# Kernel optimization log

Measured on AMD Instinct MI355X. Metric: run time of the kernel, lower is better.

The kernel has to match this reference:

```python
import jax, jax.numpy as jnp
import numpy as np

N, B, NPG = 65536, 512, 128      # total nodes, graphs, nodes per graph
E, EPG = 524288, 1024            # total edges, edges per graph
D, R, L = 64, 16, 3              # emb_dim, num relations, encoder layers
PHI = 0.1
EPS_VAR = 1e-5


def _mean_std(x):
    # torch.var is unbiased (ddof=1); keep last-dim stats per row
    m = jnp.mean(x, axis=-1, keepdims=True)
    s = jnp.sqrt(jnp.var(x, axis=-1, ddof=1, keepdims=True) + EPS_VAR)
    return m, s


def _rgcn_encode(feat, Wrel, Wself, b, src, dst, etype, edge_w):
    """L-layer relational GCN. Returns (last_h [N,D], repr [N,L,D])."""
    h = feat
    reps = []
    for l in range(L):
        hr = jnp.einsum('nd,rdk->nrk', h, Wrel[l])        # [N,R,D]
        msg = hr[src, etype]                               # [E,D] per-edge typed transform
        msg = msg * edge_w[:, None]
        agg = jax.ops.segment_sum(msg, dst, num_segments=N)
        deg = jax.ops.segment_sum(edge_w, dst, num_segments=N)
        h = jax.nn.relu(h @ Wself[l] + agg / jnp.clip(deg, 1.0)[:, None] + b[l])
        reps.append(h)
    return h, jnp.stack(reps, axis=1)


def _pool(rep, node_gid):
    # mean_nodes over 'repr': graphs have fixed NPG nodes
    s = jax.ops.segment_sum(rep.reshape(N, L * D), node_gid, num_segments=B)
    return (s / NPG).reshape(B, L, D)


def full_forward(feat, rel_feat, rel_proj_W, rel_proj_b, rgcn_Wrel, rgcn_Wself,
                 rgcn_b, enc_W_mean, enc_W_std, dec_Wh, dec_bh, dec_Wt, dec_bt,
                 dec_Wr, dec_br, fc_W, fc_b, eps,
                 src, dst, etype, aug_src, aug_dst, aug_etype, node_gid, rel_labels):
    ones_e = jnp.ones((E,), feat.dtype)
    # relation encoder + projection
    emb_rel = jax.nn.relu(rel_feat @ rel_proj_W + rel_proj_b)          # [R,D]
    # encode original and augmented graphs
    x, rep_g = _rgcn_encode(feat, rgcn_Wrel, rgcn_Wself, rgcn_b, src, dst, etype, ones_e)
    g_out = _pool(rep_g, node_gid)
    aug_x, rep_aug = _rgcn_encode(feat, rgcn_Wrel, rgcn_Wself, rgcn_b, aug_src, aug_dst, aug_etype, ones_e)
    aug_g_out = _pool(rep_aug, node_gid)
    # AdaIn style transfer (args.interp == False)
    mc, sc = _mean_std(x)
    ms, ss = _mean_std(aug_x)
    style_applied = ss * ((x - mc) / sc) + ms
    # VAE reparameterization
    z_mean = style_applied @ enc_W_mean
    z_std = style_applied @ enc_W_std
    z = z_mean + jnp.sqrt(jnp.exp(z_std)) * eps
    # decoder: edge-level DistMult scoring -> edge mask
    head_e = jax.nn.relu(z[src] @ dec_Wh + dec_bh)                     # [E,D]
    tail_e = jax.nn.relu(z[dst] @ dec_Wt + dec_bt)
    rel_e = jax.nn.relu(emb_rel[etype] @ dec_Wr + dec_br)
    logit = jnp.sum(head_e * rel_e * tail_e, axis=-1)                  # [E]
    mask = (logit >= 0.5).astype(feat.dtype)
    # root edge (edge_ids(0,1)) = first edge of each graph, forced kept
    mask = mask.at[jnp.arange(B) * EPG].set(1.0)
    # re-encode reconstructed (masked) graph with original features
    x_recon, rep_recon = _rgcn_encode(feat, rgcn_Wrel, rgcn_Wself, rgcn_b, src, dst, etype, mask)
    recon_g_out = _pool(rep_recon, node_gid)
    # head node (id==1) = node 0 of each graph; tail (id==2) = node 1
    head_ids = jnp.arange(B) * NPG
    tail_ids = head_ids + 1
    g_rep = jnp.concatenate([
        recon_g_out.reshape(B, L * D),
        rep_recon[head_ids].reshape(B, L * D),
        rep_recon[tail_ids].reshape(B, L * D),
        emb_rel[rel_labels],
    ], axis=1)                                                          # [B, 3*L*D + D]
    output = g_rep @ fc_W + fc_b                                        # [B,1]
    # reconstruction + style losses, summed over layers
    mse_per_layer = jnp.mean((rep_recon - rep_g) ** 2, axis=(0, 2))     # [L]
    mr, sr = _mean_std(rep_recon.transpose(1, 0, 2))                    # [L,N,1]
    mg, sg = _mean_std(rep_g.transpose(1, 0, 2))
    style_per_layer = jnp.mean((mr - mg) ** 2, axis=(1, 2)) + jnp.mean((sr - sg) ** 2, axis=(1, 2))
    loss = jnp.sum(mse_per_layer) + PHI * jnp.sum(style_per_layer)
    return output, g_out, aug_g_out, loss


def setup_inputs() -> dict:
    key = jax.random.key(0)
    ks = jax.random.split(key, 28)
    egid = jnp.arange(E, dtype=jnp.int32) // EPG
    node_gid = jnp.arange(N, dtype=jnp.int32) // NPG
    mk_edges = lambda k1, k2: (egid * NPG + jax.random.randint(k1, (E,), 0, NPG, jnp.int32),
                               egid * NPG + jax.random.randint(k2, (E,), 0, NPG, jnp.int32))
    src, dst = mk_edges(ks[0], ks[1])
    aug_src, aug_dst = mk_edges(ks[2], ks[3])
    g = lambda i, shape, s=0.05: (jax.random.normal(ks[i], shape, jnp.float32) * s)
    return {
        'feat': g(4, (N, D), 1.0),
        'rel_feat': g(5, (R, 64), 1.0),
        'rel_proj_W': g(6, (64, D)),
        'rel_proj_b': jnp.zeros((D,), jnp.float32),
        'rgcn_Wrel': g(7, (L, R, D, D)),
        'rgcn_Wself': g(8, (L, D, D)),
        'rgcn_b': jnp.zeros((L, D), jnp.float32),
        'enc_W_mean': g(9, (D, D)),
        'enc_W_std': g(10, (D, D)),
        'dec_Wh': g(11, (D, D), 0.1),
        'dec_bh': jnp.zeros((D,), jnp.float32),
        'dec_Wt': g(12, (D, D), 0.1),
        'dec_bt': jnp.zeros((D,), jnp.float32),
        'dec_Wr': g(13, (D, D), 0.1),
        'dec_br': jnp.zeros((D,), jnp.float32),
        'fc_W': g(14, (3 * L * D + D, 1)),
        'fc_b': jnp.zeros((1,), jnp.float32),
        'eps': g(15, (N, D), 1.0),
        'src': src, 'dst': dst,
        'etype': jax.random.randint(ks[16], (E,), 0, R, jnp.int32),
        'aug_src': aug_src, 'aug_dst': aug_dst,
        'aug_etype': jax.random.randint(ks[17], (E,), 0, R, jnp.int32),
        'node_gid': node_gid,
        'rel_labels': jax.random.randint(ks[18], (B,), 0, R, jnp.int32),
    }


def reference(feat, rel_feat, rel_proj_W, rel_proj_b, rgcn_Wrel, rgcn_Wself,
              rgcn_b, enc_W_mean, enc_W_std, dec_Wh, dec_bh, dec_Wt, dec_bt,
              dec_Wr, dec_br, fc_W, fc_b, eps,
              src, dst, etype, aug_src, aug_dst, aug_etype, node_gid, rel_labels):
    return full_forward(feat, rel_feat, rel_proj_W, rel_proj_b, rgcn_Wrel, rgcn_Wself,
                        rgcn_b, enc_W_mean, enc_W_std, dec_Wh, dec_bh, dec_Wt, dec_bt,
                        dec_Wr, dec_br, fc_W, fc_b, eps,
                        src, dst, etype, aug_src, aug_dst, aug_etype, node_gid, rel_labels)
```

## Files before the change

kernel.cpp:

```cpp
#include <hip/hip_runtime.h>
#include <hip/hip_bf16.h>

typedef __attribute__((ext_vector_type(8))) short bf16x8;
typedef __attribute__((ext_vector_type(4))) float f32x4;

#define NPG  128
#define EPG  1024
#define BG   512
#define NT   512
#define NW   8
#define PHI  0.1f
#define EPSV 1e-5f
#define SB   72
#define SF   65

#define OUT_G    512
#define OUT_AUG  98816
#define OUT_LOSS 197120
#define WS_EMB   0
#define WS_RELE  1024
#define WS_REPG  2048

__device__ __forceinline__ unsigned short f2bf(float x) {
  __hip_bfloat16 h = __float2bfloat16(x);
  return *reinterpret_cast<unsigned short*>(&h);
}
__device__ __forceinline__ float bf2f(unsigned short u) {
  __hip_bfloat16 h = *reinterpret_cast<__hip_bfloat16*>(&u);
  return __bfloat162float(h);
}
__device__ __forceinline__ void split_write(unsigned short* hh, unsigned short* hl,
                                            int idx, float x) {
  unsigned short hi = f2bf(x);
  hh[idx] = hi;
  hl[idx] = f2bf(x - bf2f(hi));
}

#define LOAD_BF(Wp, ctn, ks, bhv, blv)                                         \
  {                                                                            \
    bf16x8 h_, l_;                                                             \
    _Pragma("unroll") for (int j_ = 0; j_ < 8; j_++) {                         \
      float w_ = (Wp)[((ks) * 32 + kg * 8 + j_) * 64 + (ctn) * 16 + n];        \
      unsigned short hi_ = f2bf(w_);                                           \
      h_[j_] = (short)hi_;                                                     \
      l_[j_] = (short)f2bf(w_ - bf2f(hi_));                                    \
    }                                                                          \
    bhv = h_;                                                                  \
    blv = l_;                                                                  \
  }

__device__ __forceinline__ f32x4 mfma3(bf16x8 a0h, bf16x8 a1h, bf16x8 a0l, bf16x8 a1l,
                                       bf16x8 b0h, bf16x8 b1h, bf16x8 b0l, bf16x8 b1l,
                                       f32x4 acc) {
  acc = __builtin_amdgcn_mfma_f32_16x16x32_bf16(a0h, b0h, acc, 0, 0, 0);
  acc = __builtin_amdgcn_mfma_f32_16x16x32_bf16(a1h, b1h, acc, 0, 0, 0);
  acc = __builtin_amdgcn_mfma_f32_16x16x32_bf16(a0h, b0l, acc, 0, 0, 0);
  acc = __builtin_amdgcn_mfma_f32_16x16x32_bf16(a1h, b1l, acc, 0, 0, 0);
  acc = __builtin_amdgcn_mfma_f32_16x16x32_bf16(a0l, b0h, acc, 0, 0, 0);
  acc = __builtin_amdgcn_mfma_f32_16x16x32_bf16(a1l, b1h, acc, 0, 0, 0);
  return acc;
}

__global__ __launch_bounds__(64) void k_prologue1(
    const float* __restrict__ rel_feat, const float* __restrict__ rpW,
    const float* __restrict__ rpb, float* __restrict__ ws, float* __restrict__ out) {
  int r = blockIdx.x, j = threadIdx.x;
  float s = rpb[j];
  for (int k = 0; k < 64; k++) s = fmaf(rel_feat[r * 64 + k], rpW[k * 64 + j], s);
  ws[WS_EMB + r * 64 + j] = fmaxf(s, 0.f);
  if (r == 0 && j == 0) out[OUT_LOSS] = 0.f;
}

__global__ __launch_bounds__(64) void k_prologue2(
    const float* __restrict__ dWr, const float* __restrict__ dbr,
    float* __restrict__ ws) {
  int r = blockIdx.x, j = threadIdx.x;
  float s = dbr[j];
  for (int k = 0; k < 64; k++) s = fmaf(ws[WS_EMB + r * 64 + k], dWr[k * 64 + j], s);
  ws[WS_RELE + r * 64 + j] = fmaxf(s, 0.f);
}

__device__ void build_elist(unsigned* elist, int* cnt, int* offs, int* asg, int* wload,
                            float* dinv, const unsigned* maskbits, int useMask,
                            const int* __restrict__ et_a, const int* __restrict__ src_a,
                            const int* __restrict__ dst_a, int ge, int gn, int tid) {
  if (tid < 16) cnt[tid] = 0;
  if (tid >= 128 && tid < 256) dinv[tid - 128] = 0.f;
  __syncthreads();
  for (int i = tid; i < EPG; i += NT) {
    int keep = useMask ? (int)((maskbits[i >> 5] >> (i & 31)) & 1u) : 1;
    if (keep) {
      atomicAdd(&cnt[et_a[ge + i]], 1);
      atomicAdd(&dinv[dst_a[ge + i] - gn], 1.f);
    }
  }
  __syncthreads();
  if (tid == 0) {
    int o = 0;
    for (int r = 0; r < 16; r++) { offs[r] = o; o += (cnt[r] + 15) & ~15; }
    offs[16] = o;
    for (int w = 0; w < NW; w++) wload[w] = 0;
    unsigned used = 0;
    for (int s = 0; s < 16; s++) {
      int best = 0, bc = -1;
      for (int r = 0; r < 16; r++)
        if (!((used >> r) & 1) && cnt[r] > bc) { bc = cnt[r]; best = r; }
      used |= 1u << best;
      int bw = 0;
      for (int w = 1; w < NW; w++) if (wload[w] < wload[bw]) bw = w;
      asg[best] = bw;
      wload[bw] += (bc + 15) & ~15;
    }
  }
  if (tid >= 128 && tid < 256) {
    int v = tid - 128;
    dinv[v] = 1.0f / fmaxf(dinv[v], 1.0f);
  }
  __syncthreads();
  int total = offs[16];
  for (int s = tid; s < total; s += NT) elist[s] = 128u;
  if (tid < 16) cnt[tid] = offs[tid];
  __syncthreads();
  for (int i = tid; i < EPG; i += NT) {
    int keep = useMask ? (int)((maskbits[i >> 5] >> (i & 31)) & 1u) : 1;
    if (keep) {
      int r = et_a[ge + i];
      int pos = atomicAdd(&cnt[r], 1);
      elist[pos] = ((unsigned)(src_a[ge + i] - gn) << 8) | (unsigned)(dst_a[ge + i] - gn);
    }
  }
  __syncthreads();
}

__device__ void rgcn_layer_mfma(unsigned short* hh, unsigned short* hl, float* hf32,
                                const float* dinv, const unsigned* elist,
                                const int* offs, const int* asg,
                                const float* __restrict__ Wl,
                                const float* __restrict__ Wsl,
                                const float* __restrict__ bl, int tid) {
  int lane = tid & 63, wave = tid >> 6;
  int n = lane & 15, kg = lane >> 4;
  for (int i = tid; i < NPG * SF; i += NT) hf32[i] = 0.f;
  __syncthreads();
  for (int r = 0; r < 16; r++) {
    if (asg[r] != wave) continue;
    int base = offs[r], end = offs[r + 1];
    if (base >= end) continue;
    const float* __restrict__ W = Wl + (r << 12);
#pragma unroll 1
    for (int ch = 0; ch < 2; ch++) {
      bf16x8 bh00, bh01, bl00, bl01, bh10, bh11, bl10, bl11;
      LOAD_BF(W, ch * 2 + 0, 0, bh00, bl00);
      LOAD_BF(W, ch * 2 + 0, 1, bh01, bl01);
      LOAD_BF(W, ch * 2 + 1, 0, bh10, bl10);
      LOAD_BF(W, ch * 2 + 1, 1, bh11, bl11);
      for (int tb = base; tb < end; tb += 16) {
        int srow = (int)(elist[tb + n] >> 8);
        const unsigned short* rh = hh + srow * SB;
        const unsigned short* rl = hl + srow * SB;
        bf16x8 a0h = *(const bf16x8*)(rh + kg * 8);
        bf16x8 a1h = *(const bf16x8*)(rh + 32 + kg * 8);
        bf16x8 a0l = *(const bf16x8*)(rl + kg * 8);
        bf16x8 a1l = *(const bf16x8*)(rl + 32 + kg * 8);
        f32x4 acc0 = {0.f, 0.f, 0.f, 0.f}, acc1 = {0.f, 0.f, 0.f, 0.f};
        acc0 = mfma3(a0h, a1h, a0l, a1l, bh00, bh01, bl00, bl01, acc0);
        acc1 = mfma3(a0h, a1h, a0l, a1l, bh10, bh11, bl10, bl11, acc1);
#pragma unroll
        for (int i = 0; i < 4; i++) {
          int dst = (int)(elist[tb + kg * 4 + i] & 255u);
          if (dst < 128) {
            float* hp = hf32 + dst * SF + ch * 32 + n;
            atomicAdd(hp, acc0[i]);
            atomicAdd(hp + 16, acc1[i]);
          }
        }
      }
    }
  }
  __syncthreads();
  {
    const unsigned short* rh = hh + (wave * 16 + n) * SB;
    const unsigned short* rl = hl + (wave * 16 + n) * SB;
    bf16x8 a0h = *(const bf16x8*)(rh + kg * 8);
    bf16x8 a1h = *(const bf16x8*)(rh + 32 + kg * 8);
    bf16x8 a0l = *(const bf16x8*)(rl + kg * 8);
    bf16x8 a1l = *(const bf16x8*)(rl + 32 + kg * 8);
#pragma unroll 1
    for (int ch = 0; ch < 2; ch++) {
      bf16x8 bh00, bh01, bl00, bl01, bh10, bh11, bl10, bl11;
      LOAD_BF(Wsl, ch * 2 + 0, 0, bh00, bl00);
      LOAD_BF(Wsl, ch * 2 + 0, 1, bh01, bl01);
      LOAD_BF(Wsl, ch * 2 + 1, 0, bh10, bl10);
      LOAD_BF(Wsl, ch * 2 + 1, 1, bh11, bl11);
      f32x4 acc0 = {0.f, 0.f, 0.f, 0.f}, acc1 = {0.f, 0.f, 0.f, 0.f};
      acc0 = mfma3(a0h, a1h, a0l, a1l, bh00, bh01, bl00, bl01, acc0);
      acc1 = mfma3(a0h, a1h, a0l, a1l, bh10, bh11, bl10, bl11, acc1);
#pragma unroll
      for (int i = 0; i < 4; i++) {
        int node = wave * 16 + kg * 4 + i;
        float di = dinv[node];
#pragma unroll
        for (int c = 0; c < 2; c++) {
          int col = (ch * 2 + c) * 16 + n;
          float a = c ? acc1[i] : acc0[i];
          float v = a + hf32[node * SF + col] * di + bl[col];
          v = fmaxf(v, 0.f);
          hf32[node * SF + col] = v;
          split_write(hh, hl, node * SB + col, v);
        }
      }
    }
  }
  __syncthreads();
}

__device__ void dense_mfma(const unsigned short* ah, const unsigned short* al,
                           float* hf32, unsigned short* oh, unsigned short* ol,
                           const float* __restrict__ W, const float* __restrict__ bias,
                           int mode, const float* __restrict__ epsbuf, int gn, int tid) {
  int lane = tid & 63, wave = tid >> 6;
  int n = lane & 15, kg = lane >> 4;
  const unsigned short* rh = ah + (wave * 16 + n) * SB;
  const unsigned short* rl = al + (wave * 16 + n) * SB;
  bf16x8 a0h = *(const bf16x8*)(rh + kg * 8);
  bf16x8 a1h = *(const bf16x8*)(rh + 32 + kg * 8);
  bf16x8 a0l = *(const bf16x8*)(rl + kg * 8);
  bf16x8 a1l = *(const bf16x8*)(rl + 32 + kg * 8);
#pragma unroll 1
  for (int ch = 0; ch < 2; ch++) {
    bf16x8 bh00, bh01, bl00, bl01, bh10, bh11, bl10, bl11;
    LOAD_BF(W, ch * 2 + 0, 0, bh00, bl00);
    LOAD_BF(W, ch * 2 + 0, 1, bh01, bl01);
    LOAD_BF(W, ch * 2 + 1, 0, bh10, bl10);
    LOAD_BF(W, ch * 2 + 1, 1, bh11, bl11);
    f32x4 acc0 = {0.f, 0.f, 0.f, 0.f}, acc1 = {0.f, 0.f, 0.f, 0.f};
    acc0 = mfma3(a0h, a1h, a0l, a1l, bh00, bh01, bl00, bl01, acc0);
    acc1 = mfma3(a0h, a1h, a0l, a1l, bh10, bh11, bl10, bl11, acc1);
#pragma unroll
    for (int i = 0; i < 4; i++) {
      int node = wave * 16 + kg * 4 + i;
#pragma unroll
      for (int c = 0; c < 2; c++) {
        int col = (ch * 2 + c) * 16 + n;
        float a = c ? acc1[i] : acc0[i];
        if (mode == 0) {
          hf32[node * SF + col] = a;
        } else if (mode == 2) {
          hf32[node * SF + col] += sqrtf(expf(a)) * epsbuf[(gn + node) * 64 + col];
        } else {
          a = fmaxf(a + bias[col], 0.f);
          if (oh) split_write(oh, ol, node * SB + col, a);
          else hf32[node * SF + col] = a;
        }
      }
    }
  }
  __syncthreads();
}

__device__ void pool_sf(const float* hf32, float* red, float* dst, int tid) {
  int j = tid & 63, grp = tid >> 6;
  float s = 0.f;
  for (int v = grp * 16; v < grp * 16 + 16; v++) s += hf32[v * SF + j];
  red[tid] = s;
  __syncthreads();
  if (tid < 64) {
    float t = 0.f;
#pragma unroll
    for (int w = 0; w < NW; w++) t += red[w * 64 + tid];
    dst[tid] = t * (1.f / 128.f);
  }
  __syncthreads();
}

__global__ __launch_bounds__(NT, 2) void k_mega(
    const float* __restrict__ feat, const float* __restrict__ Wrel,
    const float* __restrict__ Wself, const float* __restrict__ bvec,
    const float* __restrict__ encWm, const float* __restrict__ encWs,
    const float* __restrict__ decWh, const float* __restrict__ dbh,
    const float* __restrict__ decWt, const float* __restrict__ dbt,
    const float* __restrict__ fcW, const float* __restrict__ fcb,
    const float* __restrict__ epsbuf,
    const int* __restrict__ srcA, const int* __restrict__ dstA, const int* __restrict__ etA,
    const int* __restrict__ asrcA, const int* __restrict__ adstA, const int* __restrict__ aetA,
    const int* __restrict__ rel_labels, float* __restrict__ ws, float* __restrict__ out) {
  __shared__ __align__(16) unsigned short hh[NPG * SB];
  __shared__ __align__(16) unsigned short hl[NPG * SB];
  __shared__ __align__(16) float hf32[NPG * SF];
  __shared__ __align__(16) unsigned elist[1280];
  __shared__ float dinv[NPG];
  __shared__ float red[NT];
  __shared__ float ht[384];
  __shared__ float rgout[192];
  __shared__ unsigned maskbits[EPG / 32];
  __shared__ int cnt[16], offs[17], asg[16], wload[NW];

  int g = blockIdx.x, tid = threadIdx.x;
  int gn = g * NPG, ge = g * EPG;
  float* repg = ws + WS_REPG;

  build_elist(elist, cnt, offs, asg, wload, dinv, maskbits, 0, etA, srcA, dstA, ge, gn, tid);
  for (int i = tid; i < 8192; i += NT)
    split_write(hh, hl, (i >> 6) * SB + (i & 63), feat[gn * 64 + i]);
  __syncthreads();
  for (int l = 0; l < 3; l++) {
    rgcn_layer_mfma(hh, hl, hf32, dinv, elist, offs, asg, Wrel + l * 65536,
                    Wself + l * 4096, bvec + l * 64, tid);
    for (int i = tid; i < 8192; i += NT)
      repg[(gn + (i >> 6)) * 192 + l * 64 + (i & 63)] = hf32[(i >> 6) * SF + (i & 63)];
    pool_sf(hf32, red, out + OUT_G + g * 192 + l * 64, tid);
  }
  build_elist(elist, cnt, offs, asg, wload, dinv, maskbits, 0, aetA, asrcA, adstA, ge, gn, tid);
  for (int i = tid; i < 8192; i += NT)
    split_write(hh, hl, (i >> 6) * SB + (i & 63), feat[gn * 64 + i]);
  __syncthreads();
  for (int l = 0; l < 3; l++) {
    rgcn_layer_mfma(hh, hl, hf32, dinv, elist, offs, asg, Wrel + l * 65536,
                    Wself + l * 4096, bvec + l * 64, tid);
    pool_sf(hf32, red, out + OUT_AUG + g * 192 + l * 64, tid);
  }
  if (tid < NPG) {
    int v = tid;
    float t1 = 0.f, t2 = 0.f;
    for (int jj = 0; jj < 64; jj++) {
      int j = (v + jj) & 63;
      float y = hf32[v * SF + j];
      t1 += y; t2 += y * y;
    }
    float ms = t1 * (1.f / 64.f);
    red[v] = ms;
    red[NPG + v] = sqrtf((t2 - 64.f * ms * ms) * (1.f / 63.f) + EPSV);
  }
  __syncthreads();
  for (int i = tid; i < 8192; i += NT)
    hf32[(i >> 6) * SF + (i & 63)] = repg[(gn + (i >> 6)) * 192 + 128 + (i & 63)];
  __syncthreads();
  if (tid < NPG) {
    int v = tid;
    float s1 = 0.f, s2 = 0.f;
    for (int jj = 0; jj < 64; jj++) {
      int j = (v + jj) & 63;
      float x = hf32[v * SF + j];
      s1 += x; s2 += x * x;
    }
    float mc = s1 * (1.f / 64.f);
    float sc = sqrtf((s2 - 64.f * mc * mc) * (1.f / 63.f) + EPSV);
    float sca = red[NPG + v] / sc, ms = red[v];
    for (int jj = 0; jj < 64; jj++) {
      int j = (v + jj) & 63;
      hf32[v * SF + j] = (hf32[v * SF + j] - mc) * sca + ms;
    }
  }
  __syncthreads();
  for (int i = tid; i < 8192; i += NT)
    split_write(hh, hl, (i >> 6) * SB + (i & 63), hf32[(i >> 6) * SF + (i & 63)]);
  __syncthreads();
  dense_mfma(hh, hl, hf32, nullptr, nullptr, encWm, nullptr, 0, nullptr, gn, tid);
  dense_mfma(hh, hl, hf32, nullptr, nullptr, encWs, nullptr, 2, epsbuf, gn, tid);
  for (int i = tid; i < 8192; i += NT)
    split_write(hh, hl, (i >> 6) * SB + (i & 63), hf32[(i >> 6) * SF + (i & 63)]);
  __syncthreads();
  dense_mfma(hh, hl, hf32, nullptr, nullptr, decWt, dbt, 1, nullptr, gn, tid);
  dense_mfma(hh, hl, hf32, hh, hl, decWh, dbh, 1, nullptr, gn, tid);
  float* relEl = (float*)elist;
  for (int i = tid; i < 1024; i += NT) relEl[i] = ws[WS_RELE + i];
  for (int i = tid; i < EPG / 32; i += NT) maskbits[i] = 0u;
  __syncthreads();
  for (int i = tid; i < EPG; i += NT) {
    int s = srcA[ge + i] - gn, t = dstA[ge + i] - gn, r = etA[ge + i];
    int rot = (s + t) & 63;
    float lg = 0.f;
    for (int jj = 0; jj < 64; jj++) {
      int j = (rot + jj) & 63;
      float zhv = bf2f(hh[s * SB + j]) + bf2f(hl[s * SB + j]);
      lg = fmaf(zhv * hf32[t * SF + j], relEl[(r << 6) + j], lg);
    }
    if (lg >= 0.5f) atomicOr(&maskbits[i >> 5], 1u << (i & 31));
  }
  __syncthreads();
  if (tid == 0) maskbits[0] |= 1u;
  __syncthreads();
  build_elist(elist, cnt, offs, asg, wload, dinv, maskbits, 1, etA, srcA, dstA, ge, gn, tid);
  for (int i = tid; i < 8192; i += NT)
    split_write(hh, hl, (i >> 6) * SB + (i & 63), feat[gn * 64 + i]);
  __syncthreads();
  const float c1 = 1.0f / (65536.0f * 64.0f);
  const float c2 = PHI / 65536.0f;
  for (int l = 0; l < 3; l++) {
    rgcn_layer_mfma(hh, hl, hf32, dinv, elist, offs, asg, Wrel + l * 65536,
                    Wself + l * 4096, bvec + l * 64, tid);
    pool_sf(hf32, red, rgout + l * 64, tid);
    if (tid < 128)
      ht[(l * 2 + (tid >> 6)) * 64 + (tid & 63)] = hf32[(tid >> 6) * SF + (tid & 63)];
    {
      int v = tid >> 2, q = tid & 3;
      const float* gp = repg + (gn + v) * 192 + l * 64 + q * 16;
      const float* hp = hf32 + v * SF + q * 16;
      float mse = 0.f, a1 = 0.f, a2 = 0.f, b1 = 0.f, b2 = 0.f;
#pragma unroll
      for (int u = 0; u < 16; u++) {
        float rc = hp[u];
        float gg = gp[u];
        float d = rc - gg;
        mse += d * d; a1 += rc; a2 += rc * rc; b1 += gg; b2 += gg * gg;
      }
#pragma unroll
      for (int m = 1; m < 4; m <<= 1) {
        mse += __shfl_xor(mse, m); a1 += __shfl_xor(a1, m); a2 += __shfl_xor(a2, m);
        b1 += __shfl_xor(b1, m); b2 += __shfl_xor(b2, m);
      }
      if (q == 0) {
        float mr = a1 * (1.f / 64.f), mg = b1 * (1.f / 64.f);
        float sr = sqrtf((a2 - 64.f * mr * mr) * (1.f / 63.f) + EPSV);
        float sg = sqrtf((b2 - 64.f * mg * mg) * (1.f / 63.f) + EPSV);
        float style = (mr - mg) * (mr - mg) + (sr - sg) * (sr - sg);
        red[v] = mse * c1 + style * c2;
      }
    }
    __syncthreads();
    if (tid < 64) {
      float x = red[tid] + red[tid + 64];
#pragma unroll
      for (int o = 32; o > 0; o >>= 1) x += __shfl_down(x, o);
      if (tid == 0) atomicAdd(&out[OUT_LOSS], x);
    }
    __syncthreads();
  }
  if (tid < 64) {
    int rl = rel_labels[g];
    const float* emb = ws + WS_EMB + rl * 64;
    float s = 0.f;
    for (int p = 0; p < 10; p++) {
      int i = p * 64 + tid;
      float gr;
      if (i < 192) gr = rgout[i];
      else if (i < 384) { int i2 = i - 192; gr = ht[((i2 >> 6) * 2 + 0) * 64 + (i2 & 63)]; }
      else if (i < 576) { int i2 = i - 384; gr = ht[((i2 >> 6) * 2 + 1) * 64 + (i2 & 63)]; }
      else gr = emb[i - 576];
      s = fmaf(gr, fcW[i], s);
    }
#pragma unroll
    for (int o = 32; o > 0; o >>= 1) s += __shfl_down(s, o);
    if (tid == 0) out[g] = s + fcb[0];
  }
}

extern "C" void kernel_launch(void* const* d_in, const int* in_sizes, int n_in,
                              void* d_out, int out_size, void* d_ws, size_t ws_size,
                              hipStream_t stream) {
  const float* feat     = (const float*)d_in[0];
  const float* rel_feat = (const float*)d_in[1];
  const float* rpW      = (const float*)d_in[2];
  const float* rpb      = (const float*)d_in[3];
  const float* Wrel     = (const float*)d_in[4];
  const float* Wself    = (const float*)d_in[5];
  const float* bvec     = (const float*)d_in[6];
  const float* encWm    = (const float*)d_in[7];
  const float* encWs    = (const float*)d_in[8];
  const float* decWh    = (const float*)d_in[9];
  const float* dbh      = (const float*)d_in[10];
  const float* decWt    = (const float*)d_in[11];
  const float* dbt      = (const float*)d_in[12];
  const float* decWr    = (const float*)d_in[13];
  const float* dbr      = (const float*)d_in[14];
  const float* fcW      = (const float*)d_in[15];
  const float* fcb      = (const float*)d_in[16];
  const float* epsb     = (const float*)d_in[17];
  const int* srcA  = (const int*)d_in[18];
  const int* dstA  = (const int*)d_in[19];
  const int* etA   = (const int*)d_in[20];
  const int* asrcA = (const int*)d_in[21];
  const int* adstA = (const int*)d_in[22];
  const int* aetA  = (const int*)d_in[23];
  const int* rel_labels = (const int*)d_in[25];
  float* out = (float*)d_out;
  float* ws  = (float*)d_ws;

  k_prologue1<<<16, 64, 0, stream>>>(rel_feat, rpW, rpb, ws, out);
  k_prologue2<<<16, 64, 0, stream>>>(decWr, dbr, ws);
  k_mega<<<BG, NT, 0, stream>>>(feat, Wrel, Wself, bvec, encWm, encWs, decWh, dbh,
                                decWt, dbt, fcW, fcb, epsb, srcA, dstA, etA,
                                asrcA, adstA, aetA, rel_labels, ws, out);
}
```

Before: 1.526 ms.

## Move split-bf16 node features from LDS to global workspace and raise occupancy

The hi/lo bf16 feature buffers are taken out of shared memory and stored instead as packed 32-bit words in a per-graph global workspace region. Fragments are loaded with vector loads and unpacked in registers. This cuts LDS use per block so launch bounds can ask for 4 blocks per CU instead of 2. In exchange, the gathers of source-node rows now go through global memory and cache rather than LDS, which adds latency on the scattered accesses, and the tighter launch bound may force register spills.

```diff
diff --git a/kernel.cpp b/kernel.cpp
--- a/kernel.cpp
+++ b/kernel.cpp
@@ -3,6 +3,7 @@
 
 typedef __attribute__((ext_vector_type(8))) short bf16x8;
 typedef __attribute__((ext_vector_type(4))) float f32x4;
+typedef __attribute__((ext_vector_type(4))) unsigned uint4v;
 
 #define NPG  128
 #define EPG  1024
@@ -11,7 +12,6 @@
 #define NW   8
 #define PHI  0.1f
 #define EPSV 1e-5f
-#define SB   72
 #define SF   65
 
 #define OUT_G    512
@@ -19,7 +19,8 @@
 #define OUT_LOSS 197120
 #define WS_EMB   0
 #define WS_RELE  1024
-#define WS_REPG  2048
+#define WS_HW    2048
+#define WS_REPG  (2048 + 65536 * 64)
 
 __device__ __forceinline__ unsigned short f2bf(float x) {
   __hip_bfloat16 h = __float2bfloat16(x);
@@ -29,11 +30,23 @@
   __hip_bfloat16 h = *reinterpret_cast<__hip_bfloat16*>(&u);
   return __bfloat162float(h);
 }
-__device__ __forceinline__ void split_write(unsigned short* hh, unsigned short* hl,
-                                            int idx, float x) {
+__device__ __forceinline__ unsigned packsw(float x) {
   unsigned short hi = f2bf(x);
-  hh[idx] = hi;
-  hl[idx] = f2bf(x - bf2f(hi));
+  unsigned short lo = f2bf(x - bf2f(hi));
+  return ((unsigned)hi << 16) | (unsigned)lo;
+}
+__device__ __forceinline__ float unpackf(unsigned u) {
+  return bf2f((unsigned short)(u >> 16)) + bf2f((unsigned short)(u & 0xffffu));
+}
+__device__ __forceinline__ void unpack_frag(const unsigned* p, bf16x8& ah, bf16x8& al) {
+  uint4v u0 = *(const uint4v*)(p);
+  uint4v u1 = *(const uint4v*)(p + 4);
+  unsigned uu[8] = {u0.x, u0.y, u0.z, u0.w, u1.x, u1.y, u1.z, u1.w};
+#pragma unroll
+  for (int j = 0; j < 8; j++) {
+    ah[j] = (short)(uu[j] >> 16);
+    al[j] = (short)(uu[j] & 0xffffu);
+  }
 }
 
 #define LOAD_BF(Wp, ctn, ks, bhv, blv)                                         \
@@ -70,7 +83,6 @@
   ws[WS_EMB + r * 64 + j] = fmaxf(s, 0.f);
   if (r == 0 && j == 0) out[OUT_LOSS] = 0.f;
 }
-
 __global__ __launch_bounds__(64) void k_prologue2(
     const float* __restrict__ dWr, const float* __restrict__ dbr,
     float* __restrict__ ws) {
@@ -132,7 +144,7 @@
   __syncthreads();
 }
 
-__device__ void rgcn_layer_mfma(unsigned short* hh, unsigned short* hl, float* hf32,
+__device__ void rgcn_layer_mfma(unsigned* hw, float* hf32,
                                 const float* dinv, const unsigned* elist,
                                 const int* offs, const int* asg,
                                 const float* __restrict__ Wl,
@@ -156,12 +168,10 @@
       LOAD_BF(W, ch * 2 + 1, 1, bh11, bl11);
       for (int tb = base; tb < end; tb += 16) {
         int srow = (int)(elist[tb + n] >> 8);
-        const unsigned short* rh = hh + srow * SB;
-        const unsigned short* rl = hl + srow * SB;
-        bf16x8 a0h = *(const bf16x8*)(rh + kg * 8);
-        bf16x8 a1h = *(const bf16x8*)(rh + 32 + kg * 8);
-        bf16x8 a0l = *(const bf16x8*)(rl + kg * 8);
-        bf16x8 a1l = *(const bf16x8*)(rl + 32 + kg * 8);
+        const unsigned* hp = hw + srow * 64;
+        bf16x8 a0h, a0l, a1h, a1l;
+        unpack_frag(hp + kg * 8, a0h, a0l);
+        unpack_frag(hp + 32 + kg * 8, a1h, a1l);
         f32x4 acc0 = {0.f, 0.f, 0.f, 0.f}, acc1 = {0.f, 0.f, 0.f, 0.f};
         acc0 = mfma3(a0h, a1h, a0l, a1l, bh00, bh01, bl00, bl01, acc0);
         acc1 = mfma3(a0h, a1h, a0l, a1l, bh10, bh11, bl10, bl11, acc1);
@@ -169,9 +179,9 @@
         for (int i = 0; i < 4; i++) {
           int dst = (int)(elist[tb + kg * 4 + i] & 255u);
           if (dst < 128) {
-            float* hp = hf32 + dst * SF + ch * 32 + n;
-            atomicAdd(hp, acc0[i]);
-            atomicAdd(hp + 16, acc1[i]);
+            float* hp2 = hf32 + dst * SF + ch * 32 + n;
+            atomicAdd(hp2, acc0[i]);
+            atomicAdd(hp2 + 16, acc1[i]);
           }
         }
       }
@@ -179,12 +189,10 @@
   }
   __syncthreads();
   {
-    const unsigned short* rh = hh + (wave * 16 + n) * SB;
-    const unsigned short* rl = hl + (wave * 16 + n) * SB;
-    bf16x8 a0h = *(const bf16x8*)(rh + kg * 8);
-    bf16x8 a1h = *(const bf16x8*)(rh + 32 + kg * 8);
-    bf16x8 a0l = *(const bf16x8*)(rl + kg * 8);
-    bf16x8 a1l = *(const bf16x8*)(rl + 32 + kg * 8);
+    const unsigned* hp = hw + (wave * 16 + n) * 64;
+    bf16x8 a0h, a0l, a1h, a1l;
+    unpack_frag(hp + kg * 8, a0h, a0l);
+    unpack_frag(hp + 32 + kg * 8, a1h, a1l);
 #pragma unroll 1
     for (int ch = 0; ch < 2; ch++) {
       bf16x8 bh00, bh01, bl00, bl01, bh10, bh11, bl10, bl11;
@@ -206,7 +214,7 @@
           float v = a + hf32[node * SF + col] * di + bl[col];
           v = fmaxf(v, 0.f);
           hf32[node * SF + col] = v;
-          split_write(hh, hl, node * SB + col, v);
+          hw[node * 64 + col] = packsw(v);
         }
       }
     }
@@ -214,18 +222,15 @@
   __syncthreads();
 }
 
-__device__ void dense_mfma(const unsigned short* ah, const unsigned short* al,
-                           float* hf32, unsigned short* oh, unsigned short* ol,
+__device__ void dense_mfma(const unsigned* hwA, float* hf32, unsigned* hwO,
                            const float* __restrict__ W, const float* __restrict__ bias,
                            int mode, const float* __restrict__ epsbuf, int gn, int tid) {
   int lane = tid & 63, wave = tid >> 6;
   int n = lane & 15, kg = lane >> 4;
-  const unsigned short* rh = ah + (wave * 16 + n) * SB;
-  const unsigned short* rl = al + (wave * 16 + n) * SB;
-  bf16x8 a0h = *(const bf16x8*)(rh + kg * 8);
-  bf16x8 a1h = *(const bf16x8*)(rh + 32 + kg * 8);
-  bf16x8 a0l = *(const bf16x8*)(rl + kg * 8);
-  bf16x8 a1l = *(const bf16x8*)(rl + 32 + kg * 8);
+  const unsigned* hp = hwA + (wave * 16 + n) * 64;
+  bf16x8 a0h, a0l, a1h, a1l;
+  unpack_frag(hp + kg * 8, a0h, a0l);
+  unpack_frag(hp + 32 + kg * 8, a1h, a1l);
 #pragma unroll 1
   for (int ch = 0; ch < 2; ch++) {
     bf16x8 bh00, bh01, bl00, bl01, bh10, bh11, bl10, bl11;
@@ -249,7 +254,7 @@
           hf32[node * SF + col] += sqrtf(expf(a)) * epsbuf[(gn + node) * 64 + col];
         } else {
           a = fmaxf(a + bias[col], 0.f);
-          if (oh) split_write(oh, ol, node * SB + col, a);
+          if (hwO) hwO[node * 64 + col] = packsw(a);
           else hf32[node * SF + col] = a;
         }
       }
@@ -273,7 +278,7 @@
   __syncthreads();
 }
 
-__global__ __launch_bounds__(NT, 2) void k_mega(
+__global__ __launch_bounds__(NT, 4) void k_mega(
     const float* __restrict__ feat, const float* __restrict__ Wrel,
     const float* __restrict__ Wself, const float* __restrict__ bvec,
     const float* __restrict__ encWm, const float* __restrict__ encWs,
@@ -284,8 +289,6 @@
     const int* __restrict__ srcA, const int* __restrict__ dstA, const int* __restrict__ etA,
     const int* __restrict__ asrcA, const int* __restrict__ adstA, const int* __restrict__ aetA,
     const int* __restrict__ rel_labels, float* __restrict__ ws, float* __restrict__ out) {
-  __shared__ __align__(16) unsigned short hh[NPG * SB];
-  __shared__ __align__(16) unsigned short hl[NPG * SB];
   __shared__ __align__(16) float hf32[NPG * SF];
   __shared__ __align__(16) unsigned elist[1280];
   __shared__ float dinv[NPG];
@@ -298,24 +301,23 @@
   int g = blockIdx.x, tid = threadIdx.x;
   int gn = g * NPG, ge = g * EPG;
   float* repg = ws + WS_REPG;
+  unsigned* hw = (unsigned*)ws + WS_HW + gn * 64;
 
   build_elist(elist, cnt, offs, asg, wload, dinv, maskbits, 0, etA, srcA, dstA, ge, gn, tid);
-  for (int i = tid; i < 8192; i += NT)
-    split_write(hh, hl, (i >> 6) * SB + (i & 63), feat[gn * 64 + i]);
+  for (int i = tid; i < 8192; i += NT) hw[i] = packsw(feat[gn * 64 + i]);
   __syncthreads();
   for (int l = 0; l < 3; l++) {
-    rgcn_layer_mfma(hh, hl, hf32, dinv, elist, offs, asg, Wrel + l * 65536,
+    rgcn_layer_mfma(hw, hf32, dinv, elist, offs, asg, Wrel + l * 65536,
                     Wself + l * 4096, bvec + l * 64, tid);
     for (int i = tid; i < 8192; i += NT)
       repg[(gn + (i >> 6)) * 192 + l * 64 + (i & 63)] = hf32[(i >> 6) * SF + (i & 63)];
     pool_sf(hf32, red, out + OUT_G + g * 192 + l * 64, tid);
   }
   build_elist(elist, cnt, offs, asg, wload, dinv, maskbits, 0, aetA, asrcA, adstA, ge, gn, tid);
-  for (int i = tid; i < 8192; i += NT)
-    split_write(hh, hl, (i >> 6) * SB + (i & 63), feat[gn * 64 + i]);
+  for (int i = tid; i < 8192; i += NT) hw[i] = packsw(feat[gn * 64 + i]);
   __syncthreads();
   for (int l = 0; l < 3; l++) {
-    rgcn_layer_mfma(hh, hl, hf32, dinv, elist, offs, asg, Wrel + l * 65536,
+    rgcn_layer_mfma(hw, hf32, dinv, elist, offs, asg, Wrel + l * 65536,
                     Wself + l * 4096, bvec + l * 64, tid);
     pool_sf(hf32, red, out + OUT_AUG + g * 192 + l * 64, tid);
   }
@@ -353,15 +355,15 @@
   }
   __syncthreads();
   for (int i = tid; i < 8192; i += NT)
-    split_write(hh, hl, (i >> 6) * SB + (i & 63), hf32[(i >> 6) * SF + (i & 63)]);
-  __syncthreads();
-  dense_mfma(hh, hl, hf32, nullptr, nullptr, encWm, nullptr, 0, nullptr, gn, tid);
-  dense_mfma(hh, hl, hf32, nullptr, nullptr, encWs, nullptr, 2, epsbuf, gn, tid);
+    hw[i] = packsw(hf32[(i >> 6) * SF + (i & 63)]);
+  __syncthreads();
+  dense_mfma(hw, hf32, nullptr, encWm, nullptr, 0, nullptr, gn, tid);
+  dense_mfma(hw, hf32, nullptr, encWs, nullptr, 2, epsbuf, gn, tid);
   for (int i = tid; i < 8192; i += NT)
-    split_write(hh, hl, (i >> 6) * SB + (i & 63), hf32[(i >> 6) * SF + (i & 63)]);
-  __syncthreads();
-  dense_mfma(hh, hl, hf32, nullptr, nullptr, decWt, dbt, 1, nullptr, gn, tid);
-  dense_mfma(hh, hl, hf32, hh, hl, decWh, dbh, 1, nullptr, gn, tid);
+    hw[i] = packsw(hf32[(i >> 6) * SF + (i & 63)]);
+  __syncthreads();
+  dense_mfma(hw, hf32, nullptr, decWt, dbt, 1, nullptr, gn, tid);
+  dense_mfma(hw, hf32, hw, decWh, dbh, 1, nullptr, gn, tid);
   float* relEl = (float*)elist;
   for (int i = tid; i < 1024; i += NT) relEl[i] = ws[WS_RELE + i];
   for (int i = tid; i < EPG / 32; i += NT) maskbits[i] = 0u;
@@ -372,8 +374,7 @@
     float lg = 0.f;
     for (int jj = 0; jj < 64; jj++) {
       int j = (rot + jj) & 63;
-      float zhv = bf2f(hh[s * SB + j]) + bf2f(hl[s * SB + j]);
-      lg = fmaf(zhv * hf32[t * SF + j], relEl[(r << 6) + j], lg);
+      lg = fmaf(unpackf(hw[s * 64 + j]) * hf32[t * SF + j], relEl[(r << 6) + j], lg);
     }
     if (lg >= 0.5f) atomicOr(&maskbits[i >> 5], 1u << (i & 31));
   }
@@ -381,13 +382,12 @@
   if (tid == 0) maskbits[0] |= 1u;
   __syncthreads();
   build_elist(elist, cnt, offs, asg, wload, dinv, maskbits, 1, etA, srcA, dstA, ge, gn, tid);
-  for (int i = tid; i < 8192; i += NT)
-    split_write(hh, hl, (i >> 6) * SB + (i & 63), feat[gn * 64 + i]);
+  for (int i = tid; i < 8192; i += NT) hw[i] = packsw(feat[gn * 64 + i]);
   __syncthreads();
   const float c1 = 1.0f / (65536.0f * 64.0f);
   const float c2 = PHI / 65536.0f;
   for (int l = 0; l < 3; l++) {
-    rgcn_layer_mfma(hh, hl, hf32, dinv, elist, offs, asg, Wrel + l * 65536,
+    rgcn_layer_mfma(hw, hf32, dinv, elist, offs, asg, Wrel + l * 65536,
                     Wself + l * 4096, bvec + l * 64, tid);
     pool_sf(hf32, red, rgout + l * 64, tid);
     if (tid < 128)
```

After: 1.525 ms. Within noise of the previous version (-0.1%).
